# Kernel optimization log

Measured on AMD Instinct MI355X. Metric: run time of the kernel, lower is better.

## Reference

```python
import jax, jax.numpy as jnp
import numpy as np

EPS = 1e-09


def make_spd(x):
    # x: [B1, B2, n, n] random normal -> SPD via Gram matrix + jitter
    n = x.shape[-1]
    g = jnp.einsum('...ik,...jk->...ij', x, x) / n
    return g + 1e-3 * jnp.eye(n, dtype=x.dtype)


def setup_inputs() -> dict:
    key = jax.random.key(0)
    x = jax.random.normal(key, (256, 32, 64, 64), dtype=jnp.float32)
    return {"inputs": make_spd(x)}


def reference(inputs) -> jnp.ndarray:
    # Batched matrix log of SPD matrices: V @ diag(log(relu(w)+eps)) @ V^T
    eigval, eigvecs = jnp.linalg.eigh(inputs)            # [..., n], [..., n, n]
    log_s = jnp.log(jax.nn.relu(eigval) + EPS)           # [..., n]
    # fused reconstruction: (V * log_s) @ V^T
    return jnp.einsum('...ij,...j,...kj->...ik', eigvecs, log_s, eigvecs)
```

## Files before the change

kernel.cpp:

```cpp
#include <hip/hip_runtime.h>
#include <math.h>

#define NDIM 64
#define PITCH 68
#define KC 16
#define MAXSWEEPS 20
#define WPB 4

typedef float v2f __attribute__((ext_vector_type(2)));

__device__ __forceinline__ v2f pk_fma(v2f a, v2f b, v2f c)
{
    v2f d;
    asm("v_pk_fma_f32 %0, %1, %2, %3" : "=v"(d) : "v"(a), "v"(b), "v"(c));
    return d;
}

__device__ __forceinline__ v2f pk_mul(v2f a, v2f b)
{
    v2f d;
    asm("v_pk_mul_f32 %0, %1, %2" : "=v"(d) : "v"(a), "v"(b));
    return d;
}

__global__ __launch_bounds__(WPB * 64, 3)
void logeig_jacobi_kernel(const float* __restrict__ in, float* __restrict__ out)
{
    const int wid  = threadIdx.x >> 6;
    const int lane = threadIdx.x & 63;
    const int b    = blockIdx.x * WPB + wid;
    const float* A = in  + (size_t)b * (NDIM * NDIM);
    float*       O = out + (size_t)b * (NDIM * NDIM);

    __shared__ float ldsM[WPB][KC * PITCH];
    __shared__ float ldsW[WPB][NDIM];

    v2f x2[NDIM / 2];
#pragma unroll
    for (int i = 0; i < NDIM / 2; ++i) {
        x2[i].x = A[(2 * i + 0) * NDIM + lane];
        x2[i].y = A[(2 * i + 1) * NDIM + lane];
    }

    float alpha = 0.0f;

#pragma unroll 1
    for (int sweep = 0; sweep < MAXSWEEPS; ++sweep) {
        v2f r0 = {0.f, 0.f}, r1 = {0.f, 0.f};
#pragma unroll
        for (int i = 0; i < NDIM / 2; i += 2) {
            r0 = pk_fma(x2[i],     x2[i],     r0);
            r1 = pk_fma(x2[i + 1], x2[i + 1], r1);
        }
        alpha = (r0.x + r0.y) + (r1.x + r1.y);

        bool any_big = false;
#pragma unroll 1
        for (int mi = 1; mi < NDIM; ++mi) {
            const int m    = (sweep & 1) ? (NDIM - mi) : mi;
            const int pidx = (lane ^ m) << 2;

            v2f y2[NDIM / 2];
#pragma unroll
            for (int i = 0; i < NDIM / 2; ++i) {
                y2[i].x = __int_as_float(__builtin_amdgcn_ds_bpermute(pidx, __float_as_int(x2[i].x)));
                y2[i].y = __int_as_float(__builtin_amdgcn_ds_bpermute(pidx, __float_as_int(x2[i].y)));
            }

            v2f g0 = {0.f, 0.f}, g1 = {0.f, 0.f};
#pragma unroll
            for (int i = 0; i < NDIM / 2; i += 2) {
                g0 = pk_fma(x2[i],     y2[i],     g0);
                g1 = pk_fma(x2[i + 1], y2[i + 1], g1);
            }
            const float gamma = (g0.x + g0.y) + (g1.x + g1.y);

            const float other = __int_as_float(__builtin_amdgcn_ds_bpermute(pidx, __float_as_int(alpha)));

            const bool  is_p = lane < (lane ^ m);
            const float aa = is_p ? alpha : other;
            const float bb = is_p ? other : alpha;

            any_big = any_big || ((gamma * gamma) > (1e-9f * aa * bb));

            const bool  rot = (gamma != 0.0f);
            const float w   = 2.0f * gamma;
            const float d   = bb - aa;
            const float den = fabsf(d) + __builtin_amdgcn_sqrtf(fmaf(w, w, fmaf(d, d, 1e-35f)));
            const float t   = ((d >= 0.0f) ? w : -w) * __builtin_amdgcn_rcpf(den);
            const float cc  = __builtin_amdgcn_rsqf(fmaf(t, t, 1.0f));
            const float ss  = t * cc;

            const float sgn = is_p ? -1.0f : 1.0f;
            const float c_r = rot ? cc : 1.0f;
            const float s_r = rot ? sgn * ss : 0.0f;
            const float tg  = rot ? sgn * t * gamma : 0.0f;

            v2f c2; c2.x = c_r; c2.y = c_r;
            v2f s2; s2.x = s_r; s2.y = s_r;
#pragma unroll
            for (int i = 0; i < NDIM / 2; ++i)
                x2[i] = pk_fma(c2, x2[i], pk_mul(s2, y2[i]));
            alpha += tg;
        }
        if (__ballot(any_big) == 0ull) break;
    }

    v2f f0 = {0.f, 0.f}, f1 = {0.f, 0.f};
#pragma unroll
    for (int i = 0; i < NDIM / 2; i += 2) {
        f0 = pk_fma(x2[i],     x2[i],     f0);
        f1 = pk_fma(x2[i + 1], x2[i + 1], f1);
    }
    const float af  = (f0.x + f0.y) + (f1.x + f1.y);
    const float lam = __builtin_amdgcn_sqrtf(af);
    ldsW[wid][lane] = logf(lam + 1e-9f) / af;

    v2f acc2[NDIM / 2];
#pragma unroll
    for (int i = 0; i < NDIM / 2; ++i) { acc2[i].x = 0.f; acc2[i].y = 0.f; }

#pragma unroll 1
    for (int c = 0; c < NDIM; c += KC) {
        if (lane >= c && lane < c + KC) {
            float4* row = (float4*)&ldsM[wid][(lane - c) * PITCH];
#pragma unroll
            for (int t4 = 0; t4 < NDIM / 4; ++t4)
                row[t4] = make_float4(x2[2 * t4].x, x2[2 * t4].y,
                                      x2[2 * t4 + 1].x, x2[2 * t4 + 1].y);
        }
#pragma unroll 1
        for (int kk = 0; kk < KC; ++kk) {
            const float wk  = ldsW[wid][c + kk];
            const float mlk = ldsM[wid][kk * PITCH + lane];
            const float zk  = wk * mlk;
            v2f zk2; zk2.x = zk; zk2.y = zk;
            const float4* rowk = (const float4*)&ldsM[wid][kk * PITCH];
#pragma unroll
            for (int t4 = 0; t4 < NDIM / 4; ++t4) {
                const float4 v = rowk[t4];
                v2f lo; lo.x = v.x; lo.y = v.y;
                v2f hi; hi.x = v.z; hi.y = v.w;
                acc2[2 * t4]     = pk_fma(zk2, lo, acc2[2 * t4]);
                acc2[2 * t4 + 1] = pk_fma(zk2, hi, acc2[2 * t4 + 1]);
            }
        }
    }

#pragma unroll
    for (int i = 0; i < NDIM / 2; ++i) {
        O[(2 * i + 0) * NDIM + lane] = acc2[i].x;
        O[(2 * i + 1) * NDIM + lane] = acc2[i].y;
    }
}

extern "C" void kernel_launch(void* const* d_in, const int* in_sizes, int n_in,
                              void* d_out, int out_size, void* d_ws, size_t ws_size,
                              hipStream_t stream)
{
    const float* in  = (const float*)d_in[0];
    float*       out = (float*)d_out;
    const int nmat = out_size / (NDIM * NDIM);
    hipLaunchKernelGGL(logeig_jacobi_kernel, dim3(nmat / WPB), dim3(WPB * 64), 0, stream, in, out);
}
```

Measured before the change: 5.399 ms.

## Replace ds_bpermute partner exchange with DPP, swizzle and permlane swap chains

```diff
diff --git a/kernel.cpp b/kernel.cpp
--- a/kernel.cpp
+++ b/kernel.cpp
@@ -8,6 +8,7 @@
 #define WPB 4
 
 typedef float v2f __attribute__((ext_vector_type(2)));
+typedef unsigned int uint2v __attribute__((ext_vector_type(2)));
 
 __device__ __forceinline__ v2f pk_fma(v2f a, v2f b, v2f c)
 {
@@ -23,7 +24,29 @@
     return d;
 }
 
-__global__ __launch_bounds__(WPB * 64, 3)
+#define DPP_XOR1 0xB1
+#define DPP_XOR2 0x4E
+#define DPP_XOR3 0x1B
+#define DPP_XOR7 0x141
+#define DPP_XOR8 0x128
+
+template<int CTRL>
+__device__ __forceinline__ float dppf(float v)
+{
+    return __int_as_float(__builtin_amdgcn_mov_dpp(__float_as_int(v), CTRL, 0xF, 0xF, true));
+}
+
+__device__ __forceinline__ float swz16f(float v)
+{
+    return __int_as_float(__builtin_amdgcn_ds_swizzle(__float_as_int(v), 0x401F));
+}
+
+__device__ __forceinline__ float bpermf(int pidx, float v)
+{
+    return __int_as_float(__builtin_amdgcn_ds_bpermute(pidx, __float_as_int(v)));
+}
+
+__global__ __launch_bounds__(WPB * 64, 1)
 void logeig_jacobi_kernel(const float* __restrict__ in, float* __restrict__ out)
 {
     const int wid  = threadIdx.x >> 6;
@@ -35,6 +58,46 @@
     __shared__ float ldsM[WPB][KC * PITCH];
     __shared__ float ldsW[WPB][NDIM];
 
+    bool have32 = false, have16 = false;
+    bool pickY32 = false, pickY16 = false;
+#if __has_builtin(__builtin_amdgcn_permlane32_swap)
+    {
+        uint2v r = __builtin_amdgcn_permlane32_swap((unsigned)lane, (unsigned)lane, false, false);
+        const unsigned want = (unsigned)(lane ^ 32);
+        const bool okA = (__ballot(((lane < 32) ? r.y : r.x) == want) == ~0ull);
+        const bool okC = (__ballot(((lane < 32) ? r.x : r.y) == want) == ~0ull);
+        have32  = okA || okC;
+        pickY32 = (okA == (lane < 32));
+    }
+#endif
+#if __has_builtin(__builtin_amdgcn_permlane16_swap)
+    {
+        uint2v r = __builtin_amdgcn_permlane16_swap((unsigned)lane, (unsigned)lane, false, false);
+        const unsigned want = (unsigned)(lane ^ 16);
+        const bool okA = (__ballot((((lane & 16) == 0) ? r.y : r.x) == want) == ~0ull);
+        const bool okC = (__ballot((((lane & 16) == 0) ? r.x : r.y) == want) == ~0ull);
+        have16  = okA || okC;
+        pickY16 = (okA == ((lane & 16) == 0));
+    }
+#endif
+
+    auto p32w = [&](float v) -> float {
+#if __has_builtin(__builtin_amdgcn_permlane32_swap)
+        uint2v r = __builtin_amdgcn_permlane32_swap(__float_as_uint(v), __float_as_uint(v), false, false);
+        return __uint_as_float(pickY32 ? r.y : r.x);
+#else
+        return v;
+#endif
+    };
+    auto p16w = [&](float v) -> float {
+#if __has_builtin(__builtin_amdgcn_permlane16_swap)
+        uint2v r = __builtin_amdgcn_permlane16_swap(__float_as_uint(v), __float_as_uint(v), false, false);
+        return __uint_as_float(pickY16 ? r.y : r.x);
+#else
+        return v;
+#endif
+    };
+
     v2f x2[NDIM / 2];
 #pragma unroll
     for (int i = 0; i < NDIM / 2; ++i) {
@@ -44,6 +107,23 @@
 
     float alpha = 0.0f;
 
+#define EX_STAGE(COND, OPX)                                                      \
+    if (COND) {                                                                  \
+        aex = OPX(aex);                                                          \
+        if (first) {                                                             \
+            _Pragma("unroll")                                                    \
+            for (int i = 0; i < NDIM / 2; ++i) {                                 \
+                y2[i].x = OPX(x2[i].x); y2[i].y = OPX(x2[i].y);                  \
+            }                                                                    \
+            first = false;                                                       \
+        } else {                                                                 \
+            _Pragma("unroll")                                                    \
+            for (int i = 0; i < NDIM / 2; ++i) {                                 \
+                y2[i].x = OPX(y2[i].x); y2[i].y = OPX(y2[i].y);                  \
+            }                                                                    \
+        }                                                                        \
+    }
+
 #pragma unroll 1
     for (int sweep = 0; sweep < MAXSWEEPS; ++sweep) {
         v2f r0 = {0.f, 0.f}, r1 = {0.f, 0.f};
@@ -57,14 +137,33 @@
         bool any_big = false;
 #pragma unroll 1
         for (int mi = 1; mi < NDIM; ++mi) {
-            const int m    = (sweep & 1) ? (NDIM - mi) : mi;
-            const int pidx = (lane ^ m) << 2;
-
-            v2f y2[NDIM / 2];
-#pragma unroll
-            for (int i = 0; i < NDIM / 2; ++i) {
-                y2[i].x = __int_as_float(__builtin_amdgcn_ds_bpermute(pidx, __float_as_int(x2[i].x)));
-                y2[i].y = __int_as_float(__builtin_amdgcn_ds_bpermute(pidx, __float_as_int(x2[i].y)));
+            const int m = (sweep & 1) ? (NDIM - mi) : mi;
+
+            v2f  y2[NDIM / 2];
+            float aex = alpha;
+            bool  first = true;
+            const bool useBperm = ((m & 32) != 0) && !have32;
+            if (useBperm) {
+                const int pidx = (lane ^ m) << 2;
+#pragma unroll
+                for (int i = 0; i < NDIM / 2; ++i) {
+                    y2[i].x = bpermf(pidx, x2[i].x);
+                    y2[i].y = bpermf(pidx, x2[i].y);
+                }
+                aex = bpermf(pidx, alpha);
+                first = false;
+            } else {
+                const int  lo = m & 15;
+                const bool u7 = (lo & 4) != 0;
+                const int  r2 = (u7 ? (lo ^ 7) : lo) & 3;
+                EX_STAGE((m & 32) != 0, p32w)
+                EX_STAGE(((m & 16) != 0) && have16, p16w)
+                EX_STAGE(((m & 16) != 0) && !have16, swz16f)
+                EX_STAGE((lo & 8) != 0, dppf<DPP_XOR8>)
+                EX_STAGE(u7,            dppf<DPP_XOR7>)
+                EX_STAGE(r2 == 3,       dppf<DPP_XOR3>)
+                EX_STAGE(r2 == 2,       dppf<DPP_XOR2>)
+                EX_STAGE(r2 == 1,       dppf<DPP_XOR1>)
             }
 
             v2f g0 = {0.f, 0.f}, g1 = {0.f, 0.f};
@@ -75,11 +174,9 @@
             }
             const float gamma = (g0.x + g0.y) + (g1.x + g1.y);
 
-            const float other = __int_as_float(__builtin_amdgcn_ds_bpermute(pidx, __float_as_int(alpha)));
-
             const bool  is_p = lane < (lane ^ m);
-            const float aa = is_p ? alpha : other;
-            const float bb = is_p ? other : alpha;
+            const float aa = is_p ? alpha : aex;
+            const float bb = is_p ? aex : alpha;
 
             any_big = any_big || ((gamma * gamma) > (1e-9f * aa * bb));
 
```

Result: slower. 15.83 ms (+193.1%).
